# Performance work log

Hardware: AMD Instinct MI355X
Metric: run time of the kernel (lower is better)

## Reference

```python
import jax, jax.numpy as jnp
import numpy as np

K = 5  # kernel_size


def _unfold(x, k):
    """Torch F.unfold equivalent: [B,C,H,W] -> [B,C,k*k,H,W].
    Patch index is row-major over the kxk window (dy*k+dx), matching
    F.unfold's channel-major / window-row-major layout after view(B,C,k*k,H,W)."""
    p = k // 2
    B, C, H, W = x.shape
    xp = jnp.pad(x, ((0, 0), (0, 0), (p, p), (p, p)))
    patches = [xp[:, :, dy:dy + H, dx:dx + W] for dy in range(k) for dx in range(k)]
    return jnp.stack(patches, axis=2)


def _conv2d(x, w, b, pad):
    y = jax.lax.conv_general_dilated(
        x, w, window_strides=(1, 1), padding=[(pad, pad), (pad, pad)],
        dimension_numbers=("NCHW", "OIHW", "NCHW"))
    return y + b[None, :, None, None]


def setup_inputs() -> dict:
    key = jax.random.key(0)
    k0, k1, k2 = jax.random.split(key, 3)
    B, H, W = 2, 1024, 1024
    flow = jax.random.normal(k0, (B, 2, H, W), jnp.float32)
    # kernel_gen params: Conv2d(3,32,3,pad=1) -> ReLU -> Conv2d(32,50,1)
    w1 = jax.random.normal(k1, (32, 3, 3, 3), jnp.float32) * 0.1
    b1 = jnp.zeros((32,), jnp.float32)
    w2 = jax.random.normal(k2, (K * K * 2, 32, 1, 1), jnp.float32) * 0.1
    b2 = jnp.zeros((K * K * 2,), jnp.float32)
    return {"flow": flow, "w1": w1, "b1": b1, "w2": w2, "b2": b2}


def reference(flow, w1, b1, w2, b2):
    B, _, H, W = flow.shape
    patches = _unfold(flow, K)                       # [B,2,25,H,W]
    # torch .var(dim=2) defaults to unbiased (ddof=1)
    var = jnp.var(patches, axis=2, ddof=1)           # [B,2,H,W]
    consistency = jnp.exp(-jnp.sqrt(jnp.sum(var * var, axis=1, keepdims=True)))  # [B,1,H,W]
    guidance = jnp.concatenate([flow, consistency], axis=1)  # [B,3,H,W]
    h = jax.nn.relu(_conv2d(guidance, w1, b1, pad=1))        # [B,32,H,W]
    kernels = _conv2d(h, w2, b2, pad=0).reshape(B, 2, K * K, H, W)
    refined = jnp.sum(kernels * patches, axis=2)             # [B,2,H,W]
    return refined
```

## Files before the change

### kernel.cpp

```cpp
#include <hip/hip_runtime.h>
#include <math.h>

#define KSZ 5
#define TSX 16
#define TSY 64
#define HALO 3
#define FWX 22
#define FH  70
#define SCH 66
#define PITCH 23
#define SF_C (FH*PITCH)
#define SC_BASE (2*SF_C)
#define SMF_TOT (SC_BASE + SCH*PITCH)

typedef __attribute__((ext_vector_type(8))) short short8_t;
typedef __attribute__((ext_vector_type(4))) float float4_t;

static __device__ __forceinline__ unsigned short f2bf(float f) {
    union { float f; unsigned int u; } v; v.f = f;
    return (unsigned short)((v.u + 0x7FFFu + ((v.u >> 16) & 1u)) >> 16);
}
static __device__ __forceinline__ unsigned int pk2t(float a, float b) {
    union { float f; unsigned int u; } ua, ub; ua.f = a; ub.f = b;
    return __builtin_amdgcn_perm(ub.u, ua.u, 0x07060302u);
}

static __device__ __forceinline__ void slot_decode(int n, int& c, int& sel, int& idx, bool& valid) {
    int g4c = (n >> 2) & 3;
    c = g4c >> 1; sel = g4c & 1;
    idx = ((n >> 4) << 2) + (n & 3);
    valid = sel ? (idx < 10) : (idx < 15);
}

static __device__ __forceinline__ int kperm(int s) {
    int sg = s >> 3, sj = s & 7;
    if (sg < 3) return sg*9 + sj;
    if (sj == 1) return 8;
    if (sj == 2) return 17;
    if (sj == 4) return 26;
    return -1;
}

static __device__ __forceinline__ int kperm2(int s) {
    int g = s >> 3, j = s & 7;
    return (j < 4) ? (g*4 + j) : (16 + g*4 + (j - 4));
}

__global__ __launch_bounds__(256)
void pack_kernel(const float* __restrict__ w1, const float* __restrict__ b1,
                 const float* __restrict__ w2, const float* __restrict__ b2,
                 unsigned short* __restrict__ wp, float* __restrict__ bp)
{
    const int tid = threadIdx.x;
    for (int i = tid; i < 6*64*8; i += 256) {
        int f = i >> 9, l = (i >> 3) & 63, j = i & 7;
        int m = l & 15, s = ((l >> 4) << 3) + j;
        float v;
        if (f < 2) {
            int k = kperm(s);
            v = (k >= 0) ? w1[(f*16 + m)*27 + k] : 0.f;
        } else {
            int n = (f - 2)*16 + m;
            int c, sel, idx; bool valid;
            slot_decode(n, c, sel, idx, valid);
            v = valid ? w2[(c*25 + sel*15 + idx)*32 + kperm2(s)] : 0.f;
        }
        wp[i] = f2bf(v);
    }
    for (int i = tid; i < 6*64*4; i += 256) {
        int f = i >> 8, l = (i >> 2) & 63, r = i & 3, g4 = l >> 4;
        float v;
        if (f < 2) v = b1[f*16 + g4*4 + r];
        else {
            int n = (f - 2)*16 + g4*4 + r;
            int c, sel, idx; bool valid;
            slot_decode(n, c, sel, idx, valid);
            v = valid ? b2[c*25 + sel*15 + idx] : 0.f;
        }
        bp[i] = v;
    }
}

__global__ __launch_bounds__(256)
void refine_kernel(const float* __restrict__ flow,
                   const unsigned short* __restrict__ wp,
                   const float* __restrict__ bp,
                   float* __restrict__ out, int H, int W)
{
    __shared__ float smf[SMF_TOT];
    __shared__ __align__(16) float4_t rs[FH*18];

    const int tid = threadIdx.x;
    const int x0 = blockIdx.x * TSX;
    const int y0 = blockIdx.y * TSY;
    const int b  = blockIdx.z;

    const int lane = tid & 63;
    const int wave = tid >> 6;
    const int col  = lane & 15;
    const int g4   = lane >> 4;

    short8_t w1A[2], w2A[4];
    float4_t cb1[2], cb2[4];
    #pragma unroll
    for (int nt = 0; nt < 2; ++nt) {
        w1A[nt] = *(const short8_t*)&wp[(nt*64 + lane)*8];
        cb1[nt] = *(const float4_t*)&bp[(nt*64 + lane)*4];
    }
    #pragma unroll
    for (int nt = 0; nt < 4; ++nt) {
        w2A[nt] = *(const short8_t*)&wp[((2+nt)*64 + lane)*8];
        cb2[nt] = *(const float4_t*)&bp[((2+nt)*64 + lane)*4];
    }

    {
        const float* srcb = flow + (size_t)(b*2) * H * W;
        if (x0 >= HALO && x0 + TSX + HALO <= W && y0 >= HALO && y0 + TSY + HALO <= H) {
            const float* s = srcb + (size_t)(y0 - HALO) * W + (x0 - HALO);
            for (int i = tid; i < 2*FH*FWX; i += 256) {
                int c = 0, r = i;
                if (r >= FH*FWX) { c = 1; r -= FH*FWX; }
                int ly = r / FWX, lx = r - ly*FWX;
                smf[c*SF_C + ly*PITCH + lx] = s[(size_t)c*H*W + ly*W + lx];
            }
        } else {
            for (int i = tid; i < 2*FH*FWX; i += 256) {
                int c = 0, r = i;
                if (r >= FH*FWX) { c = 1; r -= FH*FWX; }
                int ly = r / FWX, lx = r - ly*FWX;
                int gy = y0 - HALO + ly, gx = x0 - HALO + lx;
                float v = 0.f;
                if (gy >= 0 && gy < H && gx >= 0 && gx < W)
                    v = srcb[(size_t)c*H*W + (size_t)gy*W + gx];
                smf[c*SF_C + ly*PITCH + lx] = v;
            }
        }
    }
    __syncthreads();

    for (int i = tid; i < FH*9; i += 256) {
        int y = i / 9, xp = (i - y*9) * 2;
        const float* r0 = &smf[y*PITCH + xp];
        const float* r1 = &smf[SF_C + y*PITCH + xp];
        float a0=r0[0], a1=r0[1], a2=r0[2], a3=r0[3], a4=r0[4], a5=r0[5];
        float c0=r1[0], c1=r1[1], c2=r1[2], c3=r1[3], c4=r1[4], c5=r1[5];
        float sA = ((a0+a1)+(a2+a3))+a4;
        float qA = fmaf(a4,a4, fmaf(a3,a3, fmaf(a2,a2, fmaf(a1,a1, a0*a0))));
        float sB = ((c0+c1)+(c2+c3))+c4;
        float qB = fmaf(c4,c4, fmaf(c3,c3, fmaf(c2,c2, fmaf(c1,c1, c0*c0))));
        float sA1 = sA + a5 - a0;
        float qA1 = fmaf(-a0, a0, fmaf(a5, a5, qA));
        float sB1 = sB + c5 - c0;
        float qB1 = fmaf(-c0, c0, fmaf(c5, c5, qB));
        rs[y*18 + xp]     = (float4_t){sA,  qA,  sB,  qB };
        rs[y*18 + xp + 1] = (float4_t){sA1, qA1, sB1, qB1};
    }
    __syncthreads();

    for (int i = tid; i < SCH*18; i += 256) {
        int py = i / 18, px = i - py*18;
        int gy = y0 - 1 + py, gx = x0 - 1 + px;
        float cons = 0.f;
        if (gy >= 0 && gy < H && gx >= 0 && gx < W) {
            const float4_t* rp = rs + py*18 + px;
            float4_t acc = rp[0];
            #pragma unroll
            for (int dy = 1; dy < KSZ; ++dy) acc += rp[dy*18];
            float v0 = (acc.y - acc.x*acc.x*(1.f/25.f)) * (1.f/24.f);
            float v1 = (acc.w - acc.z*acc.z*(1.f/25.f)) * (1.f/24.f);
            cons = __expf(-sqrtf(v0*v0 + v1*v1));
        }
        smf[SC_BASE + py*PITCH + px] = cons;
    }
    __syncthreads();

    int gb0, gb1, gb2, gb3;
    {
        int ty0 = wave*16;
        int p0 = 0*SF_C + (ty0 + 2)*PITCH + (col + 2);
        int p1 = 1*SF_C + (ty0 + 2)*PITCH + (col + 2);
        int p2 = SC_BASE + ty0*PITCH + col;
        if (g4 == 0)      { gb0 = gb1 = gb2 = gb3 = p0; }
        else if (g4 == 1) { gb0 = gb1 = gb2 = gb3 = p1; }
        else if (g4 == 2) { gb0 = gb1 = gb2 = gb3 = p2; }
        else { gb0 = p0 + 47; gb1 = p1 + 46; gb2 = p2 + 24; gb3 = p0; }
    }

    const int sel = g4 & 1, pc = g4 >> 1;
    int pb = pc*SF_C + sel*(3*PITCH) + PITCH + 1 + col + (wave*16)*PITCH;
    float pv[15];
    #pragma unroll
    for (int i = 0; i < 15; ++i) pv[i] = smf[pb + (i/5)*PITCH + (i%5)];

    #pragma unroll
    for (int mt = 0; mt < 16; ++mt) {
        const int ty = wave*16 + mt;

        float ga = smf[gb0 + 0],  gbv = smf[gb0 + 1];
        float gc = smf[gb1 + 2],  gd  = smf[gb1 + 23];
        float ge = smf[gb2 + 24], gf  = smf[gb2 + 25];
        float gg = smf[gb3 + 46], gh  = smf[gb3 + 47];
        union { unsigned int u[4]; short8_t s; } gu;
        gu.u[0] = pk2t(ga, gbv); gu.u[1] = pk2t(gc, gd);
        gu.u[2] = pk2t(ge, gf);  gu.u[3] = pk2t(gg, gh);
        short8_t gB = gu.s;
        gb0 += PITCH; gb1 += PITCH; gb2 += PITCH; gb3 += PITCH;

        float4_t h0 = __builtin_amdgcn_mfma_f32_16x16x32_bf16(w1A[0], gB, cb1[0], 0, 0, 0);
        float4_t h1 = __builtin_amdgcn_mfma_f32_16x16x32_bf16(w1A[1], gB, cb1[1], 0, 0, 0);

        union { unsigned int u[4]; short8_t s; } hu;
        hu.u[0] = pk2t(fmaxf(h0[0],0.f), fmaxf(h0[1],0.f));
        hu.u[1] = pk2t(fmaxf(h0[2],0.f), fmaxf(h0[3],0.f));
        hu.u[2] = pk2t(fmaxf(h1[0],0.f), fmaxf(h1[1],0.f));
        hu.u[3] = pk2t(fmaxf(h1[2],0.f), fmaxf(h1[3],0.f));
        short8_t hf = hu.s;

        float4_t ka[4];
        #pragma unroll
        for (int nt = 0; nt < 4; ++nt)
            ka[nt] = __builtin_amdgcn_mfma_f32_16x16x32_bf16(w2A[nt], hf, cb2[nt], 0, 0, 0);

        float s = 0.f;
        #pragma unroll
        for (int i = 0; i < 15; ++i)
            s = fmaf(ka[i >> 2][i & 3], pv[i], s);

        if (mt < 15) {
            #pragma unroll
            for (int i = 0; i < 10; ++i) pv[i] = pv[i + 5];
            pb += PITCH;
            #pragma unroll
            for (int i = 10; i < 15; ++i) pv[i] = smf[pb + (i/5)*PITCH + (i%5)];
        }

        s += __shfl_xor(s, 16);

        if (sel == 0) {
            int y = y0 + ty, x = x0 + col;
            out[((size_t)(b*2 + pc) * H + y) * W + x] = s;
        }
    }
}

extern "C" void kernel_launch(void* const* d_in, const int* in_sizes, int n_in,
                              void* d_out, int out_size, void* d_ws, size_t ws_size,
                              hipStream_t stream) {
    const float* flow = (const float*)d_in[0];
    const float* w1   = (const float*)d_in[1];
    const float* b1   = (const float*)d_in[2];
    const float* w2   = (const float*)d_in[3];
    const float* b2   = (const float*)d_in[4];
    float* out = (float*)d_out;

    unsigned short* wp = (unsigned short*)d_ws;
    float* bp = (float*)((char*)d_ws + 8192);

    const int H = 1024, W = 1024;
    const int B = in_sizes[0] / (2 * H * W);

    pack_kernel<<<1, 256, 0, stream>>>(w1, b1, w2, b2, wp, bp);
    dim3 grid(W / TSX, H / TSY, B);
    refine_kernel<<<grid, dim3(256), 0, stream>>>(flow, wp, bp, out, H, W);
}
```

Measured before the change: 115.6 us.

## Interleave two independent row streams per wave and pair consistency rows

The per-wave 16-row MFMA loop is split into two independent 8-row streams, A and B, processed in the same iteration. This gives the scheduler independent MFMA chains to overlap instead of one serial dependency chain per row. The consistency pass now computes two output rows per thread and shares the four middle row-sum loads between them. Launch bounds request 4 blocks per CU, which caps register use while the second stream doubles the live patch registers, so spilling is a risk.

```diff
diff --git a/kernel.cpp b/kernel.cpp
--- a/kernel.cpp
+++ b/kernel.cpp
@@ -81,7 +81,7 @@
     }
 }
 
-__global__ __launch_bounds__(256)
+__global__ __launch_bounds__(256, 4)
 void refine_kernel(const float* __restrict__ flow,
                    const unsigned short* __restrict__ wp,
                    const float* __restrict__ bp,
@@ -157,88 +157,139 @@
     }
     __syncthreads();
 
-    for (int i = tid; i < SCH*18; i += 256) {
-        int py = i / 18, px = i - py*18;
-        int gy = y0 - 1 + py, gx = x0 - 1 + px;
-        float cons = 0.f;
-        if (gy >= 0 && gy < H && gx >= 0 && gx < W) {
-            const float4_t* rp = rs + py*18 + px;
-            float4_t acc = rp[0];
+    for (int i = tid; i < (SCH/2)*18; i += 256) {
+        int u = i / 18, px = i - u*18;
+        int py0 = u*2;
+        int gx = x0 - 1 + px;
+        int gy0 = y0 - 1 + py0;
+        const float4_t* rp = rs + py0*18 + px;
+        float4_t r0 = rp[0], r1 = rp[18], r2 = rp[2*18], r3 = rp[3*18],
+                 r4 = rp[4*18], r5 = rp[5*18];
+        float4_t mid = (r1 + r2) + (r3 + r4);
+        float4_t acc0 = mid + r0;
+        float4_t acc1 = mid + r5;
+        float cons0 = 0.f, cons1 = 0.f;
+        bool okx = (gx >= 0) && (gx < W);
+        if (okx && gy0 >= 0 && gy0 < H) {
+            float v0 = (acc0.y - acc0.x*acc0.x*(1.f/25.f)) * (1.f/24.f);
+            float v1 = (acc0.w - acc0.z*acc0.z*(1.f/25.f)) * (1.f/24.f);
+            cons0 = __expf(-sqrtf(v0*v0 + v1*v1));
+        }
+        if (okx && gy0+1 >= 0 && gy0+1 < H) {
+            float v0 = (acc1.y - acc1.x*acc1.x*(1.f/25.f)) * (1.f/24.f);
+            float v1 = (acc1.w - acc1.z*acc1.z*(1.f/25.f)) * (1.f/24.f);
+            cons1 = __expf(-sqrtf(v0*v0 + v1*v1));
+        }
+        smf[SC_BASE + py0*PITCH + px]       = cons0;
+        smf[SC_BASE + (py0+1)*PITCH + px]   = cons1;
+    }
+    __syncthreads();
+
+    const int sel = g4 & 1, pc = g4 >> 1;
+    const int tyA = wave*16, tyB = wave*16 + 8;
+
+    int gA0, gA1, gA2, gA3, gB0, gB1, gB2, gB3;
+    {
+        int p0 = 0*SF_C + 2*PITCH + (col + 2);
+        int p1 = 1*SF_C + 2*PITCH + (col + 2);
+        int p2 = SC_BASE + col;
+        int q0, q1, q2, q3;
+        if (g4 == 0)      { q0 = q1 = q2 = q3 = p0; }
+        else if (g4 == 1) { q0 = q1 = q2 = q3 = p1; }
+        else if (g4 == 2) { q0 = q1 = q2 = q3 = p2; }
+        else { q0 = p0 + 47; q1 = p1 + 46; q2 = p2 + 24; q3 = p0; }
+        gA0 = q0 + tyA*((g4==2) ? PITCH : PITCH);
+        gA0 = q0 + tyA*PITCH; gA1 = q1 + tyA*PITCH; gA2 = q2 + tyA*PITCH; gA3 = q3 + tyA*PITCH;
+        gB0 = q0 + tyB*PITCH; gB1 = q1 + tyB*PITCH; gB2 = q2 + tyB*PITCH; gB3 = q3 + tyB*PITCH;
+    }
+
+    const int pbase = pc*SF_C + sel*(3*PITCH) + PITCH + 1 + col;
+    int pbA = pbase + tyA*PITCH, pbB = pbase + tyB*PITCH;
+    float pvA[15], pvB[15];
+    #pragma unroll
+    for (int i = 0; i < 15; ++i) pvA[i] = smf[pbA + (i/5)*PITCH + (i%5)];
+    #pragma unroll
+    for (int i = 0; i < 15; ++i) pvB[i] = smf[pbB + (i/5)*PITCH + (i%5)];
+
+    #pragma unroll
+    for (int mt = 0; mt < 8; ++mt) {
+        float sA;
+        {
+            float ga = smf[gA0 + 0],  gb_ = smf[gA0 + 1];
+            float gc = smf[gA1 + 2],  gd  = smf[gA1 + 23];
+            float ge = smf[gA2 + 24], gf  = smf[gA2 + 25];
+            float gg = smf[gA3 + 46], gh  = smf[gA3 + 47];
+            union { unsigned int u[4]; short8_t s; } gu;
+            gu.u[0] = pk2t(ga, gb_); gu.u[1] = pk2t(gc, gd);
+            gu.u[2] = pk2t(ge, gf);  gu.u[3] = pk2t(gg, gh);
+            gA0 += PITCH; gA1 += PITCH; gA2 += PITCH; gA3 += PITCH;
+            float4_t h0 = __builtin_amdgcn_mfma_f32_16x16x32_bf16(w1A[0], gu.s, cb1[0], 0, 0, 0);
+            float4_t h1 = __builtin_amdgcn_mfma_f32_16x16x32_bf16(w1A[1], gu.s, cb1[1], 0, 0, 0);
+            union { unsigned int u[4]; short8_t s; } hu;
+            hu.u[0] = pk2t(fmaxf(h0[0],0.f), fmaxf(h0[1],0.f));
+            hu.u[1] = pk2t(fmaxf(h0[2],0.f), fmaxf(h0[3],0.f));
+            hu.u[2] = pk2t(fmaxf(h1[0],0.f), fmaxf(h1[1],0.f));
+            hu.u[3] = pk2t(fmaxf(h1[2],0.f), fmaxf(h1[3],0.f));
+            float4_t ka[4];
             #pragma unroll
-            for (int dy = 1; dy < KSZ; ++dy) acc += rp[dy*18];
-            float v0 = (acc.y - acc.x*acc.x*(1.f/25.f)) * (1.f/24.f);
-            float v1 = (acc.w - acc.z*acc.z*(1.f/25.f)) * (1.f/24.f);
-            cons = __expf(-sqrtf(v0*v0 + v1*v1));
-        }
-        smf[SC_BASE + py*PITCH + px] = cons;
-    }
-    __syncthreads();
-
-    int gb0, gb1, gb2, gb3;
-    {
-        int ty0 = wave*16;
-        int p0 = 0*SF_C + (ty0 + 2)*PITCH + (col + 2);
-        int p1 = 1*SF_C + (ty0 + 2)*PITCH + (col + 2);
-        int p2 = SC_BASE + ty0*PITCH + col;
-        if (g4 == 0)      { gb0 = gb1 = gb2 = gb3 = p0; }
-        else if (g4 == 1) { gb0 = gb1 = gb2 = gb3 = p1; }
-        else if (g4 == 2) { gb0 = gb1 = gb2 = gb3 = p2; }
-        else { gb0 = p0 + 47; gb1 = p1 + 46; gb2 = p2 + 24; gb3 = p0; }
-    }
-
-    const int sel = g4 & 1, pc = g4 >> 1;
-    int pb = pc*SF_C + sel*(3*PITCH) + PITCH + 1 + col + (wave*16)*PITCH;
-    float pv[15];
-    #pragma unroll
-    for (int i = 0; i < 15; ++i) pv[i] = smf[pb + (i/5)*PITCH + (i%5)];
-
-    #pragma unroll
-    for (int mt = 0; mt < 16; ++mt) {
-        const int ty = wave*16 + mt;
-
-        float ga = smf[gb0 + 0],  gbv = smf[gb0 + 1];
-        float gc = smf[gb1 + 2],  gd  = smf[gb1 + 23];
-        float ge = smf[gb2 + 24], gf  = smf[gb2 + 25];
-        float gg = smf[gb3 + 46], gh  = smf[gb3 + 47];
-        union { unsigned int u[4]; short8_t s; } gu;
-        gu.u[0] = pk2t(ga, gbv); gu.u[1] = pk2t(gc, gd);
-        gu.u[2] = pk2t(ge, gf);  gu.u[3] = pk2t(gg, gh);
-        short8_t gB = gu.s;
-        gb0 += PITCH; gb1 += PITCH; gb2 += PITCH; gb3 += PITCH;
-
-        float4_t h0 = __builtin_amdgcn_mfma_f32_16x16x32_bf16(w1A[0], gB, cb1[0], 0, 0, 0);
-        float4_t h1 = __builtin_amdgcn_mfma_f32_16x16x32_bf16(w1A[1], gB, cb1[1], 0, 0, 0);
-
-        union { unsigned int u[4]; short8_t s; } hu;
-        hu.u[0] = pk2t(fmaxf(h0[0],0.f), fmaxf(h0[1],0.f));
-        hu.u[1] = pk2t(fmaxf(h0[2],0.f), fmaxf(h0[3],0.f));
-        hu.u[2] = pk2t(fmaxf(h1[0],0.f), fmaxf(h1[1],0.f));
-        hu.u[3] = pk2t(fmaxf(h1[2],0.f), fmaxf(h1[3],0.f));
-        short8_t hf = hu.s;
-
-        float4_t ka[4];
-        #pragma unroll
-        for (int nt = 0; nt < 4; ++nt)
-            ka[nt] = __builtin_amdgcn_mfma_f32_16x16x32_bf16(w2A[nt], hf, cb2[nt], 0, 0, 0);
-
-        float s = 0.f;
-        #pragma unroll
-        for (int i = 0; i < 15; ++i)
-            s = fmaf(ka[i >> 2][i & 3], pv[i], s);
-
-        if (mt < 15) {
+            for (int nt = 0; nt < 4; ++nt)
+                ka[nt] = __builtin_amdgcn_mfma_f32_16x16x32_bf16(w2A[nt], hu.s, cb2[nt], 0, 0, 0);
+            float s = 0.f;
             #pragma unroll
-            for (int i = 0; i < 10; ++i) pv[i] = pv[i + 5];
-            pb += PITCH;
+            for (int i = 0; i < 15; ++i)
+                s = fmaf(ka[i >> 2][i & 3], pvA[i], s);
+            if (mt < 7) {
+                #pragma unroll
+                for (int i = 0; i < 10; ++i) pvA[i] = pvA[i + 5];
+                pbA += PITCH;
+                #pragma unroll
+                for (int i = 10; i < 15; ++i) pvA[i] = smf[pbA + (i/5)*PITCH + (i%5)];
+            }
+            sA = s;
+        }
+        float sB;
+        {
+            float ga = smf[gB0 + 0],  gb_ = smf[gB0 + 1];
+            float gc = smf[gB1 + 2],  gd  = smf[gB1 + 23];
+            float ge = smf[gB2 + 24], gf  = smf[gB2 + 25];
+            float gg = smf[gB3 + 46], gh  = smf[gB3 + 47];
+            union { unsigned int u[4]; short8_t s; } gu;
+            gu.u[0] = pk2t(ga, gb_); gu.u[1] = pk2t(gc, gd);
+            gu.u[2] = pk2t(ge, gf);  gu.u[3] = pk2t(gg, gh);
+            gB0 += PITCH; gB1 += PITCH; gB2 += PITCH; gB3 += PITCH;
+            float4_t h0 = __builtin_amdgcn_mfma_f32_16x16x32_bf16(w1A[0], gu.s, cb1[0], 0, 0, 0);
+            float4_t h1 = __builtin_amdgcn_mfma_f32_16x16x32_bf16(w1A[1], gu.s, cb1[1], 0, 0, 0);
+            union { unsigned int u[4]; short8_t s; } hu;
+            hu.u[0] = pk2t(fmaxf(h0[0],0.f), fmaxf(h0[1],0.f));
+            hu.u[1] = pk2t(fmaxf(h0[2],0.f), fmaxf(h0[3],0.f));
+            hu.u[2] = pk2t(fmaxf(h1[0],0.f), fmaxf(h1[1],0.f));
+            hu.u[3] = pk2t(fmaxf(h1[2],0.f), fmaxf(h1[3],0.f));
+            float4_t ka[4];
             #pragma unroll
-            for (int i = 10; i < 15; ++i) pv[i] = smf[pb + (i/5)*PITCH + (i%5)];
-        }
-
-        s += __shfl_xor(s, 16);
+            for (int nt = 0; nt < 4; ++nt)
+                ka[nt] = __builtin_amdgcn_mfma_f32_16x16x32_bf16(w2A[nt], hu.s, cb2[nt], 0, 0, 0);
+            float s = 0.f;
+            #pragma unroll
+            for (int i = 0; i < 15; ++i)
+                s = fmaf(ka[i >> 2][i & 3], pvB[i], s);
+            if (mt < 7) {
+                #pragma unroll
+                for (int i = 0; i < 10; ++i) pvB[i] = pvB[i + 5];
+                pbB += PITCH;
+                #pragma unroll
+                for (int i = 10; i < 15; ++i) pvB[i] = smf[pbB + (i/5)*PITCH + (i%5)];
+            }
+            sB = s;
+        }
+
+        sA += __shfl_xor(sA, 16);
+        sB += __shfl_xor(sB, 16);
 
         if (sel == 0) {
-            int y = y0 + ty, x = x0 + col;
-            out[((size_t)(b*2 + pc) * H + y) * W + x] = s;
+            int x = x0 + col;
+            size_t base = ((size_t)(b*2 + pc) * H) * W + x;
+            out[base + (size_t)(y0 + tyA + mt) * W] = sA;
+            out[base + (size_t)(y0 + tyB + mt) * W] = sB;
         }
     }
 }
```

After: 112.6 us. -2.6%, faster.
